# Kernel tuning notes

Measured on AMD Instinct MI355X. Metric: run time of the kernel, lower is better.

## Reference

```python
import jax, jax.numpy as jnp
import numpy as np


def _segment_mean(msg, dst, num_nodes):
    # msg: [E, B, O, T] summed into [N, B, O, T], mean over incoming edges
    s = jax.ops.segment_sum(msg, dst, num_segments=num_nodes)
    cnt = jax.ops.segment_sum(jnp.ones((msg.shape[0],), msg.dtype), dst, num_segments=num_nodes)
    return s / jnp.clip(cnt, 1.0)[:, None, None, None]


def _gcn(x, edge_index, edge_attr, A, Wk, Wr, b):
    # Edge-conditioned (spline-style) graph conv.
    # x: [B, N, Cin, T]; edge_attr: [E, 3]; Wk: [K, Cin, Cout]
    N = x.shape[1]
    src, dst = edge_index[0], edge_index[1]
    Bw = jax.nn.softmax(edge_attr @ A, axis=-1)          # [E, K] basis weights
    We = jnp.einsum('ek,kio->eio', Bw, Wk)                # [E, Cin, Cout]
    msg = jnp.einsum('beit,eio->ebot', x[:, src], We)     # [E, B, Cout, T]
    agg = _segment_mean(msg, dst, N).transpose(1, 0, 2, 3)  # [B, N, Cout, T]
    out = agg + jnp.einsum('bnit,io->bnot', x, Wr) + b[None, None, :, None]
    return jax.nn.elu(out)


def _pool(x, P, C, T):
    # x: [B, N_l, C, T] -> flatten, sparse-pool with P [N_{l+1}, N_l], unflatten
    B, N = x.shape[0], x.shape[1]
    xf = x.reshape(B, N, C * T)
    xf = jnp.einsum('mn,bnf->bmf', P, xf)
    return xf.reshape(B, P.shape[0], C, T)


def setup_inputs() -> dict:
    key = jax.random.key(0)
    ks = jax.random.split(key, 24)
    B, T = 2, 200
    N = [2048, 512, 128, 64]
    E = [16384, 8192, 2048]
    nf = [1, 8, 16, 32, 64, 128, 128]
    ld = 64

    def rn(k, shape, scale=1.0):
        return jax.random.normal(k, shape, dtype=jnp.float32) * scale

    inp = {}
    inp['x'] = rn(ks[0], (B, N[0], nf[0], T))
    inp['ei0'] = jax.random.randint(ks[1], (2, E[0]), 0, N[0])
    inp['ea0'] = jax.random.uniform(ks[2], (E[0], 3), dtype=jnp.float32)
    inp['ei1'] = jax.random.randint(ks[3], (2, E[1]), 0, N[1])
    inp['ea1'] = jax.random.uniform(ks[4], (E[1], 3), dtype=jnp.float32)
    inp['ei2'] = jax.random.randint(ks[5], (2, E[2]), 0, N[2])
    inp['ea2'] = jax.random.uniform(ks[6], (E[2], 3), dtype=jnp.float32)
    # gcn params: (A basis map, K=3 kernel weights, root weight, bias)
    inp['A1'] = rn(ks[7], (3, 3))
    inp['Wk1'] = rn(ks[8], (3, nf[0], nf[2]), 1.0 / np.sqrt(nf[0]))
    inp['Wr1'] = rn(ks[9], (nf[0], nf[2]), 1.0 / np.sqrt(nf[0]))
    inp['b1'] = jnp.zeros((nf[2],), jnp.float32)
    inp['A2'] = rn(ks[10], (3, 3))
    inp['Wk2'] = rn(ks[11], (3, nf[2], nf[3]), 1.0 / np.sqrt(nf[2]))
    inp['Wr2'] = rn(ks[12], (nf[2], nf[3]), 1.0 / np.sqrt(nf[2]))
    inp['b2'] = jnp.zeros((nf[3],), jnp.float32)
    inp['A3'] = rn(ks[13], (3, 3))
    inp['Wk3'] = rn(ks[14], (3, nf[3], nf[4]), 1.0 / np.sqrt(nf[3]))
    inp['Wr3'] = rn(ks[15], (nf[3], nf[4]), 1.0 / np.sqrt(nf[3]))
    inp['b3'] = jnp.zeros((nf[4],), jnp.float32)
    # sparse pooling projections (dense here)
    inp['P01'] = rn(ks[16], (N[1], N[0]), 1.0 / np.sqrt(N[0]))
    inp['P12'] = rn(ks[17], (N[2], N[1]), 1.0 / np.sqrt(N[1]))
    inp['P23'] = rn(ks[18], (N[3], N[2]), 1.0 / np.sqrt(N[2]))
    # 1x1 conv encoder head
    inp['fce1_w'] = rn(ks[19], (nf[4], nf[6]), 1.0 / np.sqrt(nf[4]))
    inp['fce1_b'] = jnp.zeros((nf[6],), jnp.float32)
    inp['fce2_w'] = rn(ks[20], (nf[6], ld), 1.0 / np.sqrt(nf[6]))
    inp['fce2_b'] = jnp.zeros((ld,), jnp.float32)
    return inp


def reference(x, ei0, ea0, ei1, ea1, ei2, ea2, A1, Wk1, Wr1, b1, A2, Wk2, Wr2, b2,
              A3, Wk3, Wr3, b3, P01, P12, P23, fce1_w, fce1_b, fce2_w, fce2_b):
    T = x.shape[-1]
    # level 0 -> 1
    h = _gcn(x, ei0, ea0, A1, Wk1, Wr1, b1)          # [B, N0, 16, T]
    h = _pool(h, P01, h.shape[2], T)                 # [B, N1, 16, T]
    # level 1 -> 2
    h = _gcn(h, ei1, ea1, A2, Wk2, Wr2, b2)          # [B, N1, 32, T]
    h = _pool(h, P12, h.shape[2], T)                 # [B, N2, 32, T]
    # level 2 -> 3
    h = _gcn(h, ei2, ea2, A3, Wk3, Wr3, b3)          # [B, N2, 64, T]
    h = _pool(h, P23, h.shape[2], T)                 # [B, N3, 64, T]
    # 1x1 conv encoder head (channel-wise linear over node/time grid)
    h = jax.nn.elu(jnp.einsum('bnct,co->bnot', h, fce1_w) + fce1_b[None, None, :, None])
    mu = jnp.tanh(jnp.einsum('bnct,co->bnot', h, fce2_w) + fce2_b[None, None, :, None])
    return mu  # [B, N3, latent_dim, T]
```

## Files before the change

kernel.cpp:

```cpp
#include <hip/hip_runtime.h>
#include <hip/hip_bf16.h>

using bf16 = __hip_bfloat16;
typedef unsigned short ushort_t;
typedef unsigned int uint_t;

constexpr int B = 2, T = 200;
constexpr int N0 = 2048, N1 = 512, N2 = 128, N3 = 64;
constexpr int E0 = 16384, E1 = 8192, E2 = 2048;

typedef __attribute__((ext_vector_type(8))) short bf16x8;
typedef __attribute__((ext_vector_type(4))) float f32x4;

__device__ __forceinline__ float ldx(const void* p, long i, int bf) {
  if (bf) {
    uint_t v = (uint_t)(((const ushort_t*)p)[i]) << 16;
    float f; __builtin_memcpy(&f, &v, 4); return f;
  }
  return ((const float*)p)[i];
}
__device__ __forceinline__ float rdf(const float* p) { return *p; }
__device__ __forceinline__ float rdf(const bf16* p) { return __bfloat162float(*p); }
__device__ __forceinline__ void stf(float* p, float v) { *p = v; }
__device__ __forceinline__ void stf(bf16* p, float v) { *p = __float2bfloat16(v); }
__device__ __forceinline__ ushort_t f2bfu(float v) {
  bf16 h = __float2bfloat16(v); ushort_t u; __builtin_memcpy(&u, &h, 2); return u;
}
__device__ __forceinline__ ushort_t ldbf(const bf16* p) { ushort_t u; __builtin_memcpy(&u, p, 2); return u; }
__device__ __forceinline__ ushort_t ldbf(const float* p) { return f2bfu(*p); }

__global__ void k_zero_ints(int* p, int n) {
  int i = blockIdx.x * 256 + threadIdx.x;
  if (i < n) p[i] = 0;
}

__global__ void k_probe(const ushort_t* ea, int* flag) {
  if (threadIdx.x == 0 && blockIdx.x == 0) {
    int c = 0;
    for (int i = 0; i < 128; ++i) {
      uint_t v = (uint_t)ea[i] << 16;
      float f; __builtin_memcpy(&f, &v, 4);
      if (f >= 0.f && f <= 1.0f) c++;
    }
    *flag = (c >= 120) ? 1 : 0;
  }
}

__global__ void k_cvtall(const void* x, const void* Wk1, const void* Wr1,
                         const void* Wk2, const void* Wr2,
                         const void* Wk3, const void* Wr3,
                         const void* W1h, const void* W2h,
                         const void* b1, const void* b2, const void* b3,
                         const void* b1h, const void* b2h,
                         const void* A1, const void* A2, const void* A3,
                         float* dst, const int* flagp) {
  int i = blockIdx.x * 256 + threadIdx.x;
  int bf = *flagp;
  if (i < 819200)       dst[i] = ldx(x,   i, bf);
  else if (i < 819248)  dst[i] = ldx(Wk1, i - 819200, bf);
  else if (i < 819264)  dst[i] = ldx(Wr1, i - 819248, bf);
  else if (i < 820800)  dst[i] = ldx(Wk2, i - 819264, bf);
  else if (i < 821312)  dst[i] = ldx(Wr2, i - 820800, bf);
  else if (i < 827456)  dst[i] = ldx(Wk3, i - 821312, bf);
  else if (i < 829504)  dst[i] = ldx(Wr3, i - 827456, bf);
  else if (i < 837696)  dst[i] = ldx(W1h, i - 829504, bf);
  else if (i < 845888)  dst[i] = ldx(W2h, i - 837696, bf);
  else if (i < 845904)  dst[i] = ldx(b1,  i - 845888, bf);
  else if (i < 845936)  dst[i] = ldx(b2,  i - 845904, bf);
  else if (i < 846000)  dst[i] = ldx(b3,  i - 845936, bf);
  else if (i < 846128)  dst[i] = ldx(b1h, i - 846000, bf);
  else if (i < 846192)  dst[i] = ldx(b2h, i - 846128, bf);
  else if (i < 846201)  dst[i] = ldx(A1,  i - 846192, bf);
  else if (i < 846210)  dst[i] = ldx(A2,  i - 846201, bf);
  else if (i < 846219)  dst[i] = ldx(A3,  i - 846210, bf);
}

__global__ void k_wprep(const float* wc2, const float* wc3, const float* w1h, const float* w2h,
                        ushort_t* t2, ushort_t* t3, ushort_t* t1h, ushort_t* t2h) {
  int i = blockIdx.x * 256 + threadIdx.x;
  if (i < 2048) { int o = i >> 6, c = i & 63; t2[i] = f2bfu(wc2[c * 32 + o]); }
  else if (i < 10240) { int j = i - 2048; int o = j >> 7, c = j & 127; t3[j] = f2bfu(wc3[c * 64 + o]); }
  else if (i < 18432) { int j = i - 10240; int o = j >> 6, c = j & 63; t1h[j] = f2bfu(w1h[c * 128 + o]); }
  else if (i < 26624) { int j = i - 18432; int o = j >> 7, c = j & 127; t2h[j] = f2bfu(w2h[c * 64 + o]); }
}

__global__ void k_hist3(const int* d0, const int* d1, const int* d2,
                        int* c0, int* c1, int* c2) {
  int i = blockIdx.x * 256 + threadIdx.x;
  if (i < E0) atomicAdd(&c0[d0[i]], 1);
  if (i < E1) atomicAdd(&c1[d1[i]], 1);
  if (i < E2) atomicAdd(&c2[d2[i]], 1);
}

__global__ void k_scan3(const int* c0, int* o0, int* u0,
                        const int* c1, int* o1, int* u1,
                        const int* c2, int* o2, int* u2) {
  const int* cnt; int* off; int* cur; int N;
  if (blockIdx.x == 0)      { cnt = c0; off = o0; cur = u0; N = N0; }
  else if (blockIdx.x == 1) { cnt = c1; off = o1; cur = u1; N = N1; }
  else                      { cnt = c2; off = o2; cur = u2; N = N2; }
  int tid = threadIdx.x;
  int chunk = (N + 63) >> 6;
  int base = tid * chunk;
  int s = 0;
  for (int j = 0; j < chunk; ++j) { int idx = base + j; if (idx < N) s += cnt[idx]; }
  int pre = s;
  for (int d = 1; d < 64; d <<= 1) {
    int v = __shfl_up(pre, d, 64);
    if (tid >= d) pre += v;
  }
  int run = pre - s;
  for (int j = 0; j < chunk; ++j) {
    int idx = base + j;
    if (idx < N) { off[idx] = run; cur[idx] = run; run += cnt[idx]; }
  }
  if (tid == 63) off[N] = run;
}

__global__ void k_fill3(const int* d0, int* u0, int* e0l,
                        const int* d1, int* u1, int* e1l,
                        const int* d2, int* u2, int* e2l) {
  int i = blockIdx.x * 256 + threadIdx.x;
  if (i < E0) { int p = atomicAdd(&u0[d0[i]], 1); e0l[p] = i; }
  if (i < E1) { int p = atomicAdd(&u1[d1[i]], 1); e1l[p] = i; }
  if (i < E2) { int p = atomicAdd(&u2[d2[i]], 1); e2l[p] = i; }
}

__device__ __forceinline__ void bw_one(const void* ea, int bf, const float* A,
                                       float* bw, int e) {
  float a0 = ldx(ea, e*3+0, bf), a1 = ldx(ea, e*3+1, bf), a2 = ldx(ea, e*3+2, bf);
  float l0 = a0*A[0] + a1*A[3] + a2*A[6];
  float l1 = a0*A[1] + a1*A[4] + a2*A[7];
  float l2 = a0*A[2] + a1*A[5] + a2*A[8];
  float m = fmaxf(l0, fmaxf(l1, l2));
  float x0 = expf(l0 - m), x1 = expf(l1 - m), x2 = expf(l2 - m);
  float inv = 1.0f / (x0 + x1 + x2);
  bw[e*3+0] = x0*inv; bw[e*3+1] = x1*inv; bw[e*3+2] = x2*inv;
}

__global__ void k_bw3(const void* ea0, const void* ea1, const void* ea2,
                      const float* Am, float* bw0, float* bw1, float* bw2,
                      const int* flagp) {
  int bf = *flagp;
  int i = blockIdx.x * 256 + threadIdx.x;
  if (i < E0) bw_one(ea0, bf, Am + 0,  bw0, i);
  if (i < E1) bw_one(ea1, bf, Am + 9,  bw1, i);
  if (i < E2) bw_one(ea2, bf, Am + 18, bw2, i);
}

__global__ void k_pcvt(const void* P01, const void* P12, const void* P23,
                       ushort_t* p1, ushort_t* p2, ushort_t* p3, const int* flagp) {
  int bf = *flagp;
  int i = blockIdx.x * 256 + threadIdx.x;
  if (i < 512 * 2048) p1[i] = f2bfu(ldx(P01, i, bf));
  if (i < 128 * 512)  p2[i] = f2bfu(ldx(P12, i, bf));
  if (i < 64 * 128)   p3[i] = f2bfu(ldx(P23, i, bf));
}

__global__ __launch_bounds__(256) void k_gc1(const float* x, const int* src,
    const int* off, const int* elist, const int* cnt, const float* bw,
    const float* W, const float* bias, bf16* h1) {
  __shared__ float Wl[64];
  __shared__ float bl[16];
  int tid = threadIdx.x;
  if (tid < 64) Wl[tid] = W[tid];
  if (tid < 16) bl[tid] = bias[tid];
  __syncthreads();
  int n = blockIdx.y, b = blockIdx.z;
  int t = tid;
  if (t >= T) return;
  int beg = off[n], end = off[n + 1];
  float a0 = 0.f, a1 = 0.f, a2 = 0.f;
  for (int q = beg; q < end; ++q) {
    int e = elist[q];
    int s = src[e];
    float xv = x[(b * N0 + s) * T + t];
    a0 += bw[e*3+0] * xv; a1 += bw[e*3+1] * xv; a2 += bw[e*3+2] * xv;
  }
  int c = cnt[n];
  float inv = 1.f / (float)(c > 0 ? c : 1);
  a0 *= inv; a1 *= inv; a2 *= inv;
  float xr = x[(b * N0 + n) * T + t];
  bf16* op = h1 + ((long)(b * N0 + n) * 16) * T + t;
#pragma unroll
  for (int o = 0; o < 16; ++o) {
    float v = a0 * Wl[o] + a1 * Wl[16 + o] + a2 * Wl[32 + o] + xr * Wl[48 + o] + bl[o];
    v = v > 0.f ? v : (expf(v) - 1.f);
    op[o * T] = __float2bfloat16(v);
  }
}

template<int CIN, int CPI, typename TOut>
__global__ __launch_bounds__(256) void k_gather(const float* x, const int* src,
    const int* off, const int* elist, const int* cnt, const float* bw,
    TOut* zx, int N) {
  int tx = threadIdx.x & 63, iy = threadIdx.x >> 6;
  int t = blockIdx.x * 64 + tx;
  int n = blockIdx.y, b = blockIdx.z;
  if (t >= T) return;
  int beg = off[n], end = off[n + 1];
  float acc[3][CPI];
#pragma unroll
  for (int k = 0; k < 3; ++k)
#pragma unroll
    for (int j = 0; j < CPI; ++j) acc[k][j] = 0.f;
  for (int q = beg; q < end; ++q) {
    int e = elist[q];
    int s = src[e];
    float w0 = bw[e*3+0], w1 = bw[e*3+1], w2 = bw[e*3+2];
    const float* xp = x + ((long)(b * N + s) * CIN) * T + t;
#pragma unroll
    for (int j = 0; j < CPI; ++j) {
      int i = iy * CPI + j;
      float xv = xp[i * T];
      acc[0][j] += w0 * xv; acc[1][j] += w1 * xv; acc[2][j] += w2 * xv;
    }
  }
  int c = cnt[n];
  float inv = 1.f / (float)(c > 0 ? c : 1);
  TOut* zp = zx + ((long)(b * N + n) * 4 * CIN) * T + t;
  const float* xs = x + ((long)(b * N + n) * CIN) * T + t;
#pragma unroll
  for (int j = 0; j < CPI; ++j) {
    int i = iy * CPI + j;
    stf(zp + (0 * CIN + i) * T, acc[0][j] * inv);
    stf(zp + (1 * CIN + i) * T, acc[1][j] * inv);
    stf(zp + (2 * CIN + i) * T, acc[2][j] * inv);
    stf(zp + (3 * CIN + i) * T, xs[i * T]);
  }
}

template<int C, int O, int ACT, typename TIn, int OUTM>
__global__ __launch_bounds__(256) void k_cmixm(const TIn* in, const ushort_t* Wt,
    const float* bias, void* outp, int N, const int* flagp) {
  constexpr int KG = C / 8;
  constexpr int MT = O / 16;
  __shared__ __align__(16) ushort_t Ws[O * C];
  __shared__ __align__(16) ushort_t Is[64 * C];
  int tid = threadIdx.x;
  int w = tid >> 6, l = tid & 63;
  int lf = l & 15, quad = l >> 4;
  int t0 = blockIdx.x * 64;
  int n = blockIdx.y, b = blockIdx.z;

  {
    const uint4* Wg = (const uint4*)Wt;
    for (int s = tid; s < O * KG; s += 256) {
      int o = s / KG, kg = s % KG;
      uint4 v = Wg[s];
      *(uint4*)(Ws + o * C + ((kg ^ (o & 7)) * 8)) = v;
    }
  }
  {
    const TIn* ip = in + ((long)(b * N + n) * C) * T + t0;
    int t = tid & 63;
    bool tok = (t0 + t) < T;
    for (int kg = tid >> 6; kg < KG; kg += 4) {
      ushort_t r[8];
#pragma unroll
      for (int j = 0; j < 8; ++j)
        r[j] = tok ? ldbf(ip + (kg * 8 + j) * T + t) : (ushort_t)0;
      *(uint4*)(Is + t * C + ((kg ^ (t & 7)) * 8)) = *(uint4*)r;
    }
  }
  __syncthreads();

  f32x4 acc[MT];
#pragma unroll
  for (int mt = 0; mt < MT; ++mt) acc[mt] = (f32x4){0.f, 0.f, 0.f, 0.f};
  int tr = w * 16 + lf;
#pragma unroll
  for (int kc = 0; kc < C / 32; ++kc) {
    int kg0 = kc * 4 + quad;
    bf16x8 bfr = *(const bf16x8*)(Is + tr * C + ((kg0 ^ (tr & 7)) * 8));
#pragma unroll
    for (int mt = 0; mt < MT; ++mt) {
      int o = mt * 16 + lf;
      bf16x8 afr = *(const bf16x8*)(Ws + o * C + ((kg0 ^ (o & 7)) * 8));
      acc[mt] = __builtin_amdgcn_mfma_f32_16x16x32_bf16(afr, bfr, acc[mt], 0, 0, 0);
    }
  }
  int t = t0 + w * 16 + lf;
  if (t < T) {
    long nb = (long)(b * N + n) * O;
    int bfflag = OUTM ? *flagp : 1;
#pragma unroll
    for (int mt = 0; mt < MT; ++mt) {
#pragma unroll
      for (int r = 0; r < 4; ++r) {
        int o = mt * 16 + quad * 4 + r;
        float v = acc[mt][r] + bias[o];
        if (ACT == 0) v = v > 0.f ? v : (expf(v) - 1.f);
        else          v = tanhf(v);
        long idx = (nb + o) * T + t;
        if (OUTM == 0) ((bf16*)outp)[idx] = __float2bfloat16(v);
        else if (bfflag) ((bf16*)outp)[idx] = __float2bfloat16(v);
        else ((float*)outp)[idx] = v;
      }
    }
  }
}

template<int WMT, typename TOut>
__global__ __launch_bounds__(256) void k_pool_mfma(const ushort_t* Pb, const ushort_t* h,
                                                   TOut* out, int M, int K, int F) {
  constexpr int BM = 64 * WMT;
  __shared__ __align__(16) ushort_t As[BM * 64];
  __shared__ __align__(16) ushort_t Bs[64 * 64];
  int tid = threadIdx.x;
  int w = tid >> 6, l = tid & 63;
  int lf = l & 15, quad = l >> 4;
  int f0 = blockIdx.x * 64;
  int m0 = blockIdx.y * BM;
  int b = blockIdx.z;
  f32x4 acc[WMT][4];
#pragma unroll
  for (int wt = 0; wt < WMT; ++wt)
#pragma unroll
    for (int ft = 0; ft < 4; ++ft) acc[wt][ft] = (f32x4){0.f, 0.f, 0.f, 0.f};

  for (int k0 = 0; k0 < K; k0 += 64) {
#pragma unroll
    for (int it = 0; it < BM / 32; ++it) {
      int cc = tid + 256 * it;
      int m = cc >> 3, kc = cc & 7;
      uint4 v = *(const uint4*)(Pb + (long)(m0 + m) * K + k0 + kc * 8);
      *(uint4*)(As + m * 64 + ((kc ^ (m & 7)) * 8)) = v;
    }
    {
      int f = tid & 63, kb = (tid >> 6) * 16;
      const ushort_t* hp = h + ((long)(b * K + k0 + kb)) * F + f0 + f;
      ushort_t r[16];
#pragma unroll
      for (int i = 0; i < 16; ++i) r[i] = hp[(long)i * F];
      int kc0 = kb >> 3;
      *(uint4*)(Bs + f * 64 + ((kc0 ^ (f & 7)) * 8)) = *(uint4*)&r[0];
      *(uint4*)(Bs + f * 64 + (((kc0 + 1) ^ (f & 7)) * 8)) = *(uint4*)&r[8];
    }
    __syncthreads();
#pragma unroll
    for (int ks = 0; ks < 2; ++ks) {
      int kc = ks * 4 + quad;
      bf16x8 bfr[4];
#pragma unroll
      for (int ft = 0; ft < 4; ++ft) {
        int fl = ft * 16 + lf;
        bfr[ft] = *(const bf16x8*)(Bs + fl * 64 + ((kc ^ (fl & 7)) * 8));
      }
#pragma unroll
      for (int wt = 0; wt < WMT; ++wt) {
        int ml = wt * 64 + w * 16 + lf;
        bf16x8 afr = *(const bf16x8*)(As + ml * 64 + ((kc ^ (ml & 7)) * 8));
#pragma unroll
        for (int ft = 0; ft < 4; ++ft)
          acc[wt][ft] = __builtin_amdgcn_mfma_f32_16x16x32_bf16(afr, bfr[ft], acc[wt][ft], 0, 0, 0);
      }
    }
    __syncthreads();
  }
#pragma unroll
  for (int wt = 0; wt < WMT; ++wt) {
#pragma unroll
    for (int r = 0; r < 4; ++r) {
      int m = m0 + wt * 64 + w * 16 + quad * 4 + r;
      TOut* op = out + ((long)(b * M + m)) * F + f0 + lf;
#pragma unroll
      for (int ft = 0; ft < 4; ++ft)
        stf(op + ft * 16, acc[wt][ft][r]);
    }
  }
}

extern "C" void kernel_launch(void* const* d_in, const int* in_sizes, int n_in,
                              void* d_out, int out_size, void* d_ws, size_t ws_size,
                              hipStream_t stream) {
  const int* ei0 = (const int*)d_in[1];
  const int* ei1 = (const int*)d_in[3];
  const int* ei2 = (const int*)d_in[5];

  char* base = (char*)d_ws;
  int* I = (int*)base;
  int* cnt0 = I;         int* off0 = I + 2048;  int* cur0 = I + 4112;  int* el0 = I + 6160;
  int* cnt1 = I + 22544; int* off1 = I + 23056; int* cur1 = I + 23584; int* el1 = I + 24096;
  int* cnt2 = I + 32288; int* off2 = I + 32416; int* cur2 = I + 32560; int* el2 = I + 32688;
  int* flagp = I + 40448;
  float* Fb = (float*)(base + 163840);
  float* xc  = Fb + 0;
  float* wc1 = Fb + 819200;
  float* wc2 = Fb + 819264;
  float* wc3 = Fb + 821312;
  float* w1h = Fb + 829504;
  float* w2h = Fb + 837696;
  float* bias= Fb + 845888;
  float* Am  = Fb + 846192;
  float* bw0 = Fb + 846220;
  float* bw1 = Fb + 895372;
  float* bw2 = Fb + 919948;
  ushort_t* Pb1 = (ushort_t*)(Fb + 926092);
  ushort_t* Pb2 = (ushort_t*)(Fb + 1450380);
  ushort_t* Pb3 = (ushort_t*)(Fb + 1483148);
  ushort_t* wt2  = (ushort_t*)(Fb + 1487244);
  ushort_t* wt3  = (ushort_t*)(Fb + 1488268);
  ushort_t* wt1h = (ushort_t*)(Fb + 1492364);
  ushort_t* wt2h = (ushort_t*)(Fb + 1496460);
  char* Aa = base + 8357888;
  char* Bb = base + 21465088;

  k_zero_ints<<<160, 256, 0, stream>>>(I, 40960);
  k_probe<<<1, 64, 0, stream>>>((const ushort_t*)d_in[2], flagp);
  k_cvtall<<<3306, 256, 0, stream>>>(d_in[0], d_in[8], d_in[9], d_in[12], d_in[13],
                                     d_in[16], d_in[17], d_in[22], d_in[24],
                                     d_in[10], d_in[14], d_in[18], d_in[23], d_in[25],
                                     d_in[7], d_in[11], d_in[15], Fb, flagp);
  k_hist3<<<64, 256, 0, stream>>>(ei0 + E0, ei1 + E1, ei2 + E2, cnt0, cnt1, cnt2);
  k_scan3<<<3, 64, 0, stream>>>(cnt0, off0, cur0, cnt1, off1, cur1, cnt2, off2, cur2);
  k_fill3<<<64, 256, 0, stream>>>(ei0 + E0, cur0, el0, ei1 + E1, cur1, el1, ei2 + E2, cur2, el2);
  k_bw3<<<64, 256, 0, stream>>>(d_in[2], d_in[4], d_in[6], Am, bw0, bw1, bw2, flagp);
  k_pcvt<<<4096, 256, 0, stream>>>(d_in[19], d_in[20], d_in[21], Pb1, Pb2, Pb3, flagp);
  k_wprep<<<104, 256, 0, stream>>>(wc2, wc3, w1h, w2h, wt2, wt3, wt1h, wt2h);

  k_gc1<<<dim3(1, N0, B), 256, 0, stream>>>(xc, ei0, off0, el0, cnt0, bw0, wc1, bias + 0, (bf16*)Bb);
  k_pool_mfma<2, float><<<dim3(50, 4, B), 256, 0, stream>>>(Pb1, (const ushort_t*)Bb, (float*)Aa, 512, 2048, 3200);
  k_gather<16, 4, bf16><<<dim3(4, N1, B), 256, 0, stream>>>((const float*)Aa, ei1, off1, el1, cnt1, bw1, (bf16*)Bb, N1);
  k_cmixm<64, 32, 0, bf16, 0><<<dim3(4, N1, B), 256, 0, stream>>>((const bf16*)Bb, wt2, bias + 16, Aa, N1, flagp);
  k_pool_mfma<1, float><<<dim3(100, 2, B), 256, 0, stream>>>(Pb2, (const ushort_t*)Aa, (float*)Bb, 128, 512, 6400);
  k_gather<32, 8, bf16><<<dim3(4, N2, B), 256, 0, stream>>>((const float*)Bb, ei2, off2, el2, cnt2, bw2, (bf16*)Aa, N2);
  k_cmixm<128, 64, 0, bf16, 0><<<dim3(4, N2, B), 256, 0, stream>>>((const bf16*)Aa, wt3, bias + 48, Bb, N2, flagp);
  k_pool_mfma<1, float><<<dim3(200, 1, B), 256, 0, stream>>>(Pb3, (const ushort_t*)Bb, (float*)Aa, 64, 128, 12800);
  k_cmixm<64, 128, 0, float, 0><<<dim3(4, N3, B), 256, 0, stream>>>((const float*)Aa, wt1h, bias + 112, Bb, N3, flagp);
  k_cmixm<128, 64, 1, bf16, 1><<<dim3(4, N3, B), 256, 0, stream>>>((const bf16*)Bb, wt2h, bias + 240, d_out, N3, flagp);
}
```

Before: 331.4 us.

## Fuse prep kernels, gather with channel mix, and both head layers

Merges the zeroing, probe, conversion, basis-weight, pool-matrix and weight-transpose launches into two setup kernels, and drops the separate fp32 copy of x by reading the input directly in the first conv. Each gather stage and its channel-mix MFMA become one kernel that builds the bf16 operand tile in shared memory, so the intermediate zx tensor is never written to global memory. The two head linears are fused into one kernel that keeps the hidden activations in shared memory. The first pool widens its F tile to 128. This cuts launches and global round trips, but the fused kernels use more shared memory and registers, which may lower occupancy.

```diff
diff --git a/kernel.cpp b/kernel.cpp
--- a/kernel.cpp
+++ b/kernel.cpp
@@ -11,6 +11,22 @@
 
 typedef __attribute__((ext_vector_type(8))) short bf16x8;
 typedef __attribute__((ext_vector_type(4))) float f32x4;
+
+constexpr size_t O_FLAG = 161792;
+constexpr size_t O_WC1  = 163840;
+constexpr size_t O_BIAS = 164096;
+constexpr size_t O_BW0  = 165312;
+constexpr size_t O_BW1  = 361920;
+constexpr size_t O_BW2  = 460224;
+constexpr size_t O_PB1  = 484800;
+constexpr size_t O_PB2  = 2581952;
+constexpr size_t O_PB3  = 2713024;
+constexpr size_t O_WT2  = 2729408;
+constexpr size_t O_WT3  = 2733504;
+constexpr size_t O_W1H  = 2749888;
+constexpr size_t O_W2H  = 2766272;
+constexpr size_t O_AA   = 2785280;
+constexpr size_t O_BB   = 15892480;
 
 __device__ __forceinline__ float ldx(const void* p, long i, int bf) {
   if (bf) {
@@ -19,69 +35,87 @@
   }
   return ((const float*)p)[i];
 }
-__device__ __forceinline__ float rdf(const float* p) { return *p; }
-__device__ __forceinline__ float rdf(const bf16* p) { return __bfloat162float(*p); }
 __device__ __forceinline__ void stf(float* p, float v) { *p = v; }
 __device__ __forceinline__ void stf(bf16* p, float v) { *p = __float2bfloat16(v); }
 __device__ __forceinline__ ushort_t f2bfu(float v) {
   bf16 h = __float2bfloat16(v); ushort_t u; __builtin_memcpy(&u, &h, 2); return u;
 }
-__device__ __forceinline__ ushort_t ldbf(const bf16* p) { ushort_t u; __builtin_memcpy(&u, p, 2); return u; }
-__device__ __forceinline__ ushort_t ldbf(const float* p) { return f2bfu(*p); }
-
-__global__ void k_zero_ints(int* p, int n) {
-  int i = blockIdx.x * 256 + threadIdx.x;
-  if (i < n) p[i] = 0;
-}
-
-__global__ void k_probe(const ushort_t* ea, int* flag) {
-  if (threadIdx.x == 0 && blockIdx.x == 0) {
+
+struct InPtrs {
+  const void* ea0; const void* ea1; const void* ea2;
+  const void* P01; const void* P12; const void* P23;
+  const void* Wk1; const void* Wr1; const void* Wk2; const void* Wr2;
+  const void* Wk3; const void* Wr3; const void* W1h; const void* W2h;
+  const void* b1; const void* b2; const void* b3; const void* b1h; const void* b2h;
+  const void* A1; const void* A2; const void* A3;
+};
+
+__global__ void k_setup0(int* I, const ushort_t* ea) {
+  if (blockIdx.x < 158) {
+    int i = blockIdx.x * 256 + threadIdx.x;
+    I[i] = 0;
+  } else if (threadIdx.x == 0) {
     int c = 0;
     for (int i = 0; i < 128; ++i) {
       uint_t v = (uint_t)ea[i] << 16;
       float f; __builtin_memcpy(&f, &v, 4);
       if (f >= 0.f && f <= 1.0f) c++;
     }
-    *flag = (c >= 120) ? 1 : 0;
-  }
-}
-
-__global__ void k_cvtall(const void* x, const void* Wk1, const void* Wr1,
-                         const void* Wk2, const void* Wr2,
-                         const void* Wk3, const void* Wr3,
-                         const void* W1h, const void* W2h,
-                         const void* b1, const void* b2, const void* b3,
-                         const void* b1h, const void* b2h,
-                         const void* A1, const void* A2, const void* A3,
-                         float* dst, const int* flagp) {
-  int i = blockIdx.x * 256 + threadIdx.x;
-  int bf = *flagp;
-  if (i < 819200)       dst[i] = ldx(x,   i, bf);
-  else if (i < 819248)  dst[i] = ldx(Wk1, i - 819200, bf);
-  else if (i < 819264)  dst[i] = ldx(Wr1, i - 819248, bf);
-  else if (i < 820800)  dst[i] = ldx(Wk2, i - 819264, bf);
-  else if (i < 821312)  dst[i] = ldx(Wr2, i - 820800, bf);
-  else if (i < 827456)  dst[i] = ldx(Wk3, i - 821312, bf);
-  else if (i < 829504)  dst[i] = ldx(Wr3, i - 827456, bf);
-  else if (i < 837696)  dst[i] = ldx(W1h, i - 829504, bf);
-  else if (i < 845888)  dst[i] = ldx(W2h, i - 837696, bf);
-  else if (i < 845904)  dst[i] = ldx(b1,  i - 845888, bf);
-  else if (i < 845936)  dst[i] = ldx(b2,  i - 845904, bf);
-  else if (i < 846000)  dst[i] = ldx(b3,  i - 845936, bf);
-  else if (i < 846128)  dst[i] = ldx(b1h, i - 846000, bf);
-  else if (i < 846192)  dst[i] = ldx(b2h, i - 846128, bf);
-  else if (i < 846201)  dst[i] = ldx(A1,  i - 846192, bf);
-  else if (i < 846210)  dst[i] = ldx(A2,  i - 846201, bf);
-  else if (i < 846219)  dst[i] = ldx(A3,  i - 846210, bf);
-}
-
-__global__ void k_wprep(const float* wc2, const float* wc3, const float* w1h, const float* w2h,
-                        ushort_t* t2, ushort_t* t3, ushort_t* t1h, ushort_t* t2h) {
-  int i = blockIdx.x * 256 + threadIdx.x;
-  if (i < 2048) { int o = i >> 6, c = i & 63; t2[i] = f2bfu(wc2[c * 32 + o]); }
-  else if (i < 10240) { int j = i - 2048; int o = j >> 7, c = j & 127; t3[j] = f2bfu(wc3[c * 64 + o]); }
-  else if (i < 18432) { int j = i - 10240; int o = j >> 6, c = j & 63; t1h[j] = f2bfu(w1h[c * 128 + o]); }
-  else if (i < 26624) { int j = i - 18432; int o = j >> 7, c = j & 127; t2h[j] = f2bfu(w2h[c * 64 + o]); }
+    *(int*)((char*)I + O_FLAG) = (c >= 120) ? 1 : 0;
+  }
+}
+
+__device__ __forceinline__ void bw_one(const void* ea, int bf, const void* A,
+                                       float* bw, int e) {
+  float a0 = ldx(ea, e*3+0, bf), a1 = ldx(ea, e*3+1, bf), a2 = ldx(ea, e*3+2, bf);
+  float l0 = a0*ldx(A,0,bf) + a1*ldx(A,3,bf) + a2*ldx(A,6,bf);
+  float l1 = a0*ldx(A,1,bf) + a1*ldx(A,4,bf) + a2*ldx(A,7,bf);
+  float l2 = a0*ldx(A,2,bf) + a1*ldx(A,5,bf) + a2*ldx(A,8,bf);
+  float m = fmaxf(l0, fmaxf(l1, l2));
+  float x0 = expf(l0 - m), x1 = expf(l1 - m), x2 = expf(l2 - m);
+  float inv = 1.0f / (x0 + x1 + x2);
+  bw[e*3+0] = x0*inv; bw[e*3+1] = x1*inv; bw[e*3+2] = x2*inv;
+}
+
+__global__ void k_prep(InPtrs P, char* base) {
+  int bf = *(const int*)(base + O_FLAG);
+  int bx = blockIdx.x, tid = threadIdx.x;
+  float* bw0 = (float*)(base + O_BW0);
+  float* bw1 = (float*)(base + O_BW1);
+  float* bw2 = (float*)(base + O_BW2);
+  if (bx < 64)        { bw_one(P.ea0, bf, P.A1, bw0, bx*256+tid); return; }
+  if (bx < 96)        { bw_one(P.ea1, bf, P.A2, bw1, (bx-64)*256+tid); return; }
+  if (bx < 104)       { bw_one(P.ea2, bf, P.A3, bw2, (bx-96)*256+tid); return; }
+  if (bx < 4200)      { long i = (long)(bx-104)*256+tid;
+                        ((ushort_t*)(base+O_PB1))[i] = f2bfu(ldx(P.P01, i, bf)); return; }
+  if (bx < 4456)      { int i = (bx-4200)*256+tid;
+                        ((ushort_t*)(base+O_PB2))[i] = f2bfu(ldx(P.P12, i, bf)); return; }
+  if (bx < 4488)      { int i = (bx-4456)*256+tid;
+                        ((ushort_t*)(base+O_PB3))[i] = f2bfu(ldx(P.P23, i, bf)); return; }
+  if (bx < 4496)      { int j = (bx-4488)*256+tid; int o = j>>6, c = j&63;
+                        float v = (c<48) ? ldx(P.Wk2, c*32+o, bf) : ldx(P.Wr2, (c-48)*32+o, bf);
+                        ((ushort_t*)(base+O_WT2))[j] = f2bfu(v); return; }
+  if (bx < 4528)      { int j = (bx-4496)*256+tid; int o = j>>7, c = j&127;
+                        float v = (c<96) ? ldx(P.Wk3, c*64+o, bf) : ldx(P.Wr3, (c-96)*64+o, bf);
+                        ((ushort_t*)(base+O_WT3))[j] = f2bfu(v); return; }
+  if (bx < 4560)      { int j = (bx-4528)*256+tid; int o = j>>6, c = j&63;
+                        ((ushort_t*)(base+O_W1H))[j] = f2bfu(ldx(P.W1h, c*128+o, bf)); return; }
+  if (bx < 4592)      { int j = (bx-4560)*256+tid; int o = j>>7, c = j&127;
+                        ((ushort_t*)(base+O_W2H))[j] = f2bfu(ldx(P.W2h, c*64+o, bf)); return; }
+  {
+    int i = (bx-4592)*256+tid;
+    if (i < 64) {
+      ((float*)(base+O_WC1))[i] = (i<48) ? ldx(P.Wk1, i, bf) : ldx(P.Wr1, i-48, bf);
+    } else if (i < 368) {
+      int j = i - 64; float v;
+      if (j < 16)       v = ldx(P.b1, j, bf);
+      else if (j < 48)  v = ldx(P.b2, j-16, bf);
+      else if (j < 112) v = ldx(P.b3, j-48, bf);
+      else if (j < 240) v = ldx(P.b1h, j-112, bf);
+      else              v = ldx(P.b2h, j-240, bf);
+      ((float*)(base+O_BIAS))[j] = v;
+    }
+  }
 }
 
 __global__ void k_hist3(const int* d0, const int* d1, const int* d2,
@@ -126,46 +160,16 @@
   if (i < E2) { int p = atomicAdd(&u2[d2[i]], 1); e2l[p] = i; }
 }
 
-__device__ __forceinline__ void bw_one(const void* ea, int bf, const float* A,
-                                       float* bw, int e) {
-  float a0 = ldx(ea, e*3+0, bf), a1 = ldx(ea, e*3+1, bf), a2 = ldx(ea, e*3+2, bf);
-  float l0 = a0*A[0] + a1*A[3] + a2*A[6];
-  float l1 = a0*A[1] + a1*A[4] + a2*A[7];
-  float l2 = a0*A[2] + a1*A[5] + a2*A[8];
-  float m = fmaxf(l0, fmaxf(l1, l2));
-  float x0 = expf(l0 - m), x1 = expf(l1 - m), x2 = expf(l2 - m);
-  float inv = 1.0f / (x0 + x1 + x2);
-  bw[e*3+0] = x0*inv; bw[e*3+1] = x1*inv; bw[e*3+2] = x2*inv;
-}
-
-__global__ void k_bw3(const void* ea0, const void* ea1, const void* ea2,
-                      const float* Am, float* bw0, float* bw1, float* bw2,
-                      const int* flagp) {
-  int bf = *flagp;
-  int i = blockIdx.x * 256 + threadIdx.x;
-  if (i < E0) bw_one(ea0, bf, Am + 0,  bw0, i);
-  if (i < E1) bw_one(ea1, bf, Am + 9,  bw1, i);
-  if (i < E2) bw_one(ea2, bf, Am + 18, bw2, i);
-}
-
-__global__ void k_pcvt(const void* P01, const void* P12, const void* P23,
-                       ushort_t* p1, ushort_t* p2, ushort_t* p3, const int* flagp) {
-  int bf = *flagp;
-  int i = blockIdx.x * 256 + threadIdx.x;
-  if (i < 512 * 2048) p1[i] = f2bfu(ldx(P01, i, bf));
-  if (i < 128 * 512)  p2[i] = f2bfu(ldx(P12, i, bf));
-  if (i < 64 * 128)   p3[i] = f2bfu(ldx(P23, i, bf));
-}
-
-__global__ __launch_bounds__(256) void k_gc1(const float* x, const int* src,
+__global__ __launch_bounds__(256) void k_gc1(const void* x, const int* src,
     const int* off, const int* elist, const int* cnt, const float* bw,
-    const float* W, const float* bias, bf16* h1) {
+    const float* W, const float* bias, bf16* h1, const int* flagp) {
   __shared__ float Wl[64];
   __shared__ float bl[16];
   int tid = threadIdx.x;
   if (tid < 64) Wl[tid] = W[tid];
   if (tid < 16) bl[tid] = bias[tid];
   __syncthreads();
+  int bf = *flagp;
   int n = blockIdx.y, b = blockIdx.z;
   int t = tid;
   if (t >= T) return;
@@ -174,13 +178,13 @@
   for (int q = beg; q < end; ++q) {
     int e = elist[q];
     int s = src[e];
-    float xv = x[(b * N0 + s) * T + t];
+    float xv = ldx(x, (long)(b * N0 + s) * T + t, bf);
     a0 += bw[e*3+0] * xv; a1 += bw[e*3+1] * xv; a2 += bw[e*3+2] * xv;
   }
   int c = cnt[n];
   float inv = 1.f / (float)(c > 0 ? c : 1);
   a0 *= inv; a1 *= inv; a2 *= inv;
-  float xr = x[(b * N0 + n) * T + t];
+  float xr = ldx(x, (long)(b * N0 + n) * T + t, bf);
   bf16* op = h1 + ((long)(b * N0 + n) * 16) * T + t;
 #pragma unroll
   for (int o = 0; o < 16; ++o) {
@@ -190,49 +194,11 @@
   }
 }
 
-template<int CIN, int CPI, typename TOut>
-__global__ __launch_bounds__(256) void k_gather(const float* x, const int* src,
+template<int CIN, int CPI, int O>
+__global__ __launch_bounds__(256) void k_gcm(const float* hp, const int* src,
     const int* off, const int* elist, const int* cnt, const float* bw,
-    TOut* zx, int N) {
-  int tx = threadIdx.x & 63, iy = threadIdx.x >> 6;
-  int t = blockIdx.x * 64 + tx;
-  int n = blockIdx.y, b = blockIdx.z;
-  if (t >= T) return;
-  int beg = off[n], end = off[n + 1];
-  float acc[3][CPI];
-#pragma unroll
-  for (int k = 0; k < 3; ++k)
-#pragma unroll
-    for (int j = 0; j < CPI; ++j) acc[k][j] = 0.f;
-  for (int q = beg; q < end; ++q) {
-    int e = elist[q];
-    int s = src[e];
-    float w0 = bw[e*3+0], w1 = bw[e*3+1], w2 = bw[e*3+2];
-    const float* xp = x + ((long)(b * N + s) * CIN) * T + t;
-#pragma unroll
-    for (int j = 0; j < CPI; ++j) {
-      int i = iy * CPI + j;
-      float xv = xp[i * T];
-      acc[0][j] += w0 * xv; acc[1][j] += w1 * xv; acc[2][j] += w2 * xv;
-    }
-  }
-  int c = cnt[n];
-  float inv = 1.f / (float)(c > 0 ? c : 1);
-  TOut* zp = zx + ((long)(b * N + n) * 4 * CIN) * T + t;
-  const float* xs = x + ((long)(b * N + n) * CIN) * T + t;
-#pragma unroll
-  for (int j = 0; j < CPI; ++j) {
-    int i = iy * CPI + j;
-    stf(zp + (0 * CIN + i) * T, acc[0][j] * inv);
-    stf(zp + (1 * CIN + i) * T, acc[1][j] * inv);
-    stf(zp + (2 * CIN + i) * T, acc[2][j] * inv);
-    stf(zp + (3 * CIN + i) * T, xs[i * T]);
-  }
-}
-
-template<int C, int O, int ACT, typename TIn, int OUTM>
-__global__ __launch_bounds__(256) void k_cmixm(const TIn* in, const ushort_t* Wt,
-    const float* bias, void* outp, int N, const int* flagp) {
+    const ushort_t* Wt, const float* bias, bf16* h, int N) {
+  constexpr int C = 4 * CIN;
   constexpr int KG = C / 8;
   constexpr int MT = O / 16;
   __shared__ __align__(16) ushort_t Ws[O * C];
@@ -242,32 +208,58 @@
   int lf = l & 15, quad = l >> 4;
   int t0 = blockIdx.x * 64;
   int n = blockIdx.y, b = blockIdx.z;
-
   {
     const uint4* Wg = (const uint4*)Wt;
     for (int s = tid; s < O * KG; s += 256) {
       int o = s / KG, kg = s % KG;
-      uint4 v = Wg[s];
-      *(uint4*)(Ws + o * C + ((kg ^ (o & 7)) * 8)) = v;
-    }
-  }
-  {
-    const TIn* ip = in + ((long)(b * N + n) * C) * T + t0;
-    int t = tid & 63;
-    bool tok = (t0 + t) < T;
-    for (int kg = tid >> 6; kg < KG; kg += 4) {
-      ushort_t r[8];
-#pragma unroll
-      for (int j = 0; j < 8; ++j)
-        r[j] = tok ? ldbf(ip + (kg * 8 + j) * T + t) : (ushort_t)0;
-      *(uint4*)(Is + t * C + ((kg ^ (t & 7)) * 8)) = *(uint4*)r;
-    }
+      *(uint4*)(Ws + o * C + ((kg ^ (o & 7)) * 8)) = Wg[s];
+    }
+  }
+  int tx = tid & 63, iy = tid >> 6;
+  int t = t0 + tx;
+  bool tok = t < T;
+  float acc[3][CPI], xr[CPI];
+#pragma unroll
+  for (int k = 0; k < 3; ++k)
+#pragma unroll
+    for (int j = 0; j < CPI; ++j) acc[k][j] = 0.f;
+#pragma unroll
+  for (int j = 0; j < CPI; ++j) xr[j] = 0.f;
+  float inv = 1.f;
+  if (tok) {
+    int beg = off[n], end = off[n + 1];
+    for (int q = beg; q < end; ++q) {
+      int e = elist[q];
+      int s = src[e];
+      float w0 = bw[e*3+0], w1 = bw[e*3+1], w2 = bw[e*3+2];
+      const float* xp = hp + ((long)(b * N + s) * CIN) * T + t;
+#pragma unroll
+      for (int j = 0; j < CPI; ++j) {
+        float xv = xp[(iy * CPI + j) * T];
+        acc[0][j] += w0 * xv; acc[1][j] += w1 * xv; acc[2][j] += w2 * xv;
+      }
+    }
+    int c = cnt[n];
+    inv = 1.f / (float)(c > 0 ? c : 1);
+    const float* xs = hp + ((long)(b * N + n) * CIN) * T + t;
+#pragma unroll
+    for (int j = 0; j < CPI; ++j) xr[j] = xs[(iy * CPI + j) * T];
+  }
+#pragma unroll
+  for (int j = 0; j < CPI; ++j) {
+    int i = iy * CPI + j;
+#pragma unroll
+    for (int k = 0; k < 3; ++k) {
+      int c = k * CIN + i;
+      Is[tx * C + ((c >> 3) ^ (tx & 7)) * 8 + (c & 7)] = f2bfu(acc[k][j] * inv);
+    }
+    int c = 3 * CIN + i;
+    Is[tx * C + ((c >> 3) ^ (tx & 7)) * 8 + (c & 7)] = f2bfu(xr[j]);
   }
   __syncthreads();
-
-  f32x4 acc[MT];
-#pragma unroll
-  for (int mt = 0; mt < MT; ++mt) acc[mt] = (f32x4){0.f, 0.f, 0.f, 0.f};
+  f32x4 dacc[MT];
+#pragma unroll
+  for (int mt = 0; mt < MT; ++mt) dacc[mt] = (f32x4){0.f, 0.f, 0.f, 0.f};
   int tr = w * 16 + lf;
 #pragma unroll
   for (int kc = 0; kc < C / 32; ++kc) {
@@ -277,47 +269,43 @@
     for (int mt = 0; mt < MT; ++mt) {
       int o = mt * 16 + lf;
       bf16x8 afr = *(const bf16x8*)(Ws + o * C + ((kg0 ^ (o & 7)) * 8));
-      acc[mt] = __builtin_amdgcn_mfma_f32_16x16x32_bf16(afr, bfr, acc[mt], 0, 0, 0);
-    }
-  }
-  int t = t0 + w * 16 + lf;
-  if (t < T) {
+      dacc[mt] = __builtin_amdgcn_mfma_f32_16x16x32_bf16(afr, bfr, dacc[mt], 0, 0, 0);
+    }
+  }
+  int tg = t0 + w * 16 + lf;
+  if (tg < T) {
     long nb = (long)(b * N + n) * O;
-    int bfflag = OUTM ? *flagp : 1;
 #pragma unroll
     for (int mt = 0; mt < MT; ++mt) {
 #pragma unroll
       for (int r = 0; r < 4; ++r) {
         int o = mt * 16 + quad * 4 + r;
-        float v = acc[mt][r] + bias[o];
-        if (ACT == 0) v = v > 0.f ? v : (expf(v) - 1.f);
-        else          v = tanhf(v);
-        long idx = (nb + o) * T + t;
-        if (OUTM == 0) ((bf16*)outp)[idx] = __float2bfloat16(v);
-        else if (bfflag) ((bf16*)outp)[idx] = __float2bfloat16(v);
-        else ((float*)outp)[idx] = v;
-      }
-    }
-  }
-}
-
-template<int WMT, typename TOut>
+        float v = dacc[mt][r] + bias[o];
+        v = v > 0.f ? v : (expf(v) - 1.f);
+        h[(nb + o) * T + tg] = __float2bfloat16(v);
+      }
+    }
+  }
+}
+
+template<int WMT, int FT, typename TOut>
 __global__ __launch_bounds__(256) void k_pool_mfma(const ushort_t* Pb, const ushort_t* h,
                                                    TOut* out, int M, int K, int F) {
   constexpr int BM = 64 * WMT;
+  constexpr int BN = 16 * FT;
   __shared__ __align__(16) ushort_t As[BM * 64];
-  __shared__ __align__(16) ushort_t Bs[64 * 64];
+  __shared__ __align__(16) ushort_t Bs[BN * 64];
   int tid = threadIdx.x;
   int w = tid >> 6, l = tid & 63;
   int lf = l & 15, quad = l >> 4;
-  int f0 = blockIdx.x * 64;
+  int f0 = blockIdx.x * BN;
   int m0 = blockIdx.y * BM;
   int b = blockIdx.z;
-  f32x4 acc[WMT][4];
+  f32x4 acc[WMT][FT];
 #pragma unroll
   for (int wt = 0; wt < WMT; ++wt)
 #pragma unroll
-    for (int ft = 0; ft < 4; ++ft) acc[wt][ft] = (f32x4){0.f, 0.f, 0.f, 0.f};
+    for (int ft = 0; ft < FT; ++ft) acc[wt][ft] = (f32x4){0.f, 0.f, 0.f, 0.f};
 
   for (int k0 = 0; k0 < K; k0 += 64) {
 #pragma unroll
@@ -327,8 +315,9 @@
       uint4 v = *(const uint4*)(Pb + (long)(m0 + m) * K + k0 + kc * 8);
       *(uint4*)(As + m * 64 + ((kc ^ (m & 7)) * 8)) = v;
     }
-    {
-      int f = tid & 63, kb = (tid >> 6) * 16;
+#pragma unroll
+    for (int kb = (tid / BN) * 16; kb < 64; kb += (256 / BN) * 16) {
+      int f = tid % BN;
       const ushort_t* hp = h + ((long)(b * K + k0 + kb)) * F + f0 + f;
       ushort_t r[16];
 #pragma unroll
@@ -341,9 +330,9 @@
 #pragma unroll
     for (int ks = 0; ks < 2; ++ks) {
       int kc = ks * 4 + quad;
-      bf16x8 bfr[4];
-#pragma unroll
-      for (int ft = 0; ft < 4; ++ft) {
+      bf16x8 bfr[FT];
+#pragma unroll
+      for (int ft = 0; ft < FT; ++ft) {
         int fl = ft * 16 + lf;
         bfr[ft] = *(const bf16x8*)(Bs + fl * 64 + ((kc ^ (fl & 7)) * 8));
       }
@@ -352,7 +341,7 @@
         int ml = wt * 64 + w * 16 + lf;
         bf16x8 afr = *(const bf16x8*)(As + ml * 64 + ((kc ^ (ml & 7)) * 8));
 #pragma unroll
-        for (int ft = 0; ft < 4; ++ft)
+        for (int ft = 0; ft < FT; ++ft)
           acc[wt][ft] = __builtin_amdgcn_mfma_f32_16x16x32_bf16(afr, bfr[ft], acc[wt][ft], 0, 0, 0);
       }
     }
@@ -365,8 +354,107 @@
       int m = m0 + wt * 64 + w * 16 + quad * 4 + r;
       TOut* op = out + ((long)(b * M + m)) * F + f0 + lf;
 #pragma unroll
-      for (int ft = 0; ft < 4; ++ft)
+      for (int ft = 0; ft < FT; ++ft)
         stf(op + ft * 16, acc[wt][ft][r]);
+    }
+  }
+}
+
+__global__ __launch_bounds__(256) void k_head(const float* hp3, const ushort_t* W1t,
+    const ushort_t* W2t, const float* bias, void* outp, const int* flagp) {
+  __shared__ __align__(16) ushort_t Ws1[128 * 64];
+  __shared__ __align__(16) ushort_t Ws2[64 * 128];
+  __shared__ __align__(16) ushort_t Is[64 * 64];
+  __shared__ __align__(16) ushort_t G[64 * 128];
+  int tid = threadIdx.x;
+  int w = tid >> 6, l = tid & 63;
+  int lf = l & 15, quad = l >> 4;
+  int t0 = blockIdx.x * 64;
+  int n = blockIdx.y, b = blockIdx.z;
+  {
+    const uint4* g1 = (const uint4*)W1t;
+    for (int s = tid; s < 1024; s += 256) {
+      int o = s >> 3, kg = s & 7;
+      *(uint4*)(Ws1 + o * 64 + ((kg ^ (o & 7)) * 8)) = g1[s];
+    }
+    const uint4* g2 = (const uint4*)W2t;
+    for (int s = tid; s < 1024; s += 256) {
+      int o = s >> 4, kg = s & 15;
+      *(uint4*)(Ws2 + o * 128 + ((kg ^ (o & 7)) * 8)) = g2[s];
+    }
+  }
+  {
+    int t = tid & 63;
+    bool tok = (t0 + t) < T;
+    const float* ip = hp3 + ((long)(b * 64 + n) * 64) * T + t0;
+    for (int kg = tid >> 6; kg < 8; kg += 4) {
+      ushort_t r[8];
+#pragma unroll
+      for (int j = 0; j < 8; ++j)
+        r[j] = tok ? f2bfu(ip[(kg * 8 + j) * T + t]) : (ushort_t)0;
+      *(uint4*)(Is + t * 64 + ((kg ^ (t & 7)) * 8)) = *(uint4*)r;
+    }
+  }
+  __syncthreads();
+  int tr = w * 16 + lf;
+  {
+    f32x4 a1[8];
+#pragma unroll
+    for (int mt = 0; mt < 8; ++mt) a1[mt] = (f32x4){0.f, 0.f, 0.f, 0.f};
+#pragma unroll
+    for (int kc = 0; kc < 2; ++kc) {
+      int kg0 = kc * 4 + quad;
+      bf16x8 bfr = *(const bf16x8*)(Is + tr * 64 + ((kg0 ^ (tr & 7)) * 8));
+#pragma unroll
+      for (int mt = 0; mt < 8; ++mt) {
+        int o = mt * 16 + lf;
+        bf16x8 afr = *(const bf16x8*)(Ws1 + o * 64 + ((kg0 ^ (o & 7)) * 8));
+        a1[mt] = __builtin_amdgcn_mfma_f32_16x16x32_bf16(afr, bfr, a1[mt], 0, 0, 0);
+      }
+    }
+    int tG = w * 16 + lf;
+#pragma unroll
+    for (int mt = 0; mt < 8; ++mt) {
+#pragma unroll
+      for (int r = 0; r < 4; ++r) {
+        int o1 = mt * 16 + quad * 4 + r;
+        float v = a1[mt][r] + bias[112 + o1];
+        v = v > 0.f ? v : (expf(v) - 1.f);
+        G[tG * 128 + ((o1 >> 3) ^ (tG & 7)) * 8 + (o1 & 7)] = f2bfu(v);
+      }
+    }
+  }
+  __syncthreads();
+  {
+    f32x4 a2[4];
+#pragma unroll
+    for (int mt = 0; mt < 4; ++mt) a2[mt] = (f32x4){0.f, 0.f, 0.f, 0.f};
+#pragma unroll
+    for (int kc = 0; kc < 4; ++kc) {
+      int kg0 = kc * 4 + quad;
+      bf16x8 bfr = *(const bf16x8*)(G + tr * 128 + ((kg0 ^ (tr & 7)) * 8));
+#pragma unroll
+      for (int mt = 0; mt < 4; ++mt) {
+        int o = mt * 16 + lf;
+        bf16x8 afr = *(const bf16x8*)(Ws2 + o * 128 + ((kg0 ^ (o & 7)) * 8));
+        a2[mt] = __builtin_amdgcn_mfma_f32_16x16x32_bf16(afr, bfr, a2[mt], 0, 0, 0);
+      }
+    }
+    int t = t0 + w * 16 + lf;
+    if (t < T) {
+      int bf = *flagp;
+      long nb = (long)(b * 64 + n) * 64;
+#pragma unroll
+      for (int mt = 0; mt < 4; ++mt) {
+#pragma unroll
+        for (int r = 0; r < 4; ++r) {
+          int o2 = mt * 16 + quad * 4 + r;
+          float v = tanhf(a2[mt][r] + bias[240 + o2]);
+          long idx = (nb + o2) * T + t;
+          if (bf) ((bf16*)outp)[idx] = __float2bfloat16(v);
+          else    ((float*)outp)[idx] = v;
+        }
+      }
     }
   }
 }
@@ -383,50 +471,38 @@
   int* cnt0 = I;         int* off0 = I + 2048;  int* cur0 = I + 4112;  int* el0 = I + 6160;
   int* cnt1 = I + 22544; int* off1 = I + 23056; int* cur1 = I + 23584; int* el1 = I + 24096;
   int* cnt2 = I + 32288; int* off2 = I + 32416; int* cur2 = I + 32560; int* el2 = I + 32688;
-  int* flagp = I + 40448;
-  float* Fb = (float*)(base + 163840);
-  float* xc  = Fb + 0;
-  float* wc1 = Fb + 819200;
-  float* wc2 = Fb + 819264;
-  float* wc3 = Fb + 821312;
-  float* w1h = Fb + 829504;
-  float* w2h = Fb + 837696;
-  float* bias= Fb + 845888;
-  float* Am  = Fb + 846192;
-  float* bw0 = Fb + 846220;
-  float* bw1 = Fb + 895372;
-  float* bw2 = Fb + 919948;
-  ushort_t* Pb1 = (ushort_t*)(Fb + 926092);
-  ushort_t* Pb2 = (ushort_t*)(Fb + 1450380);
-  ushort_t* Pb3 = (ushort_t*)(Fb + 1483148);
-  ushort_t* wt2  = (ushort_t*)(Fb + 1487244);
-  ushort_t* wt3  = (ushort_t*)(Fb + 1488268);
-  ushort_t* wt1h = (ushort_t*)(Fb + 1492364);
-  ushort_t* wt2h = (ushort_t*)(Fb + 1496460);
-  char* Aa = base + 8357888;
-  char* Bb = base + 21465088;
-
-  k_zero_ints<<<160, 256, 0, stream>>>(I, 40960);
-  k_probe<<<1, 64, 0, stream>>>((const ushort_t*)d_in[2], flagp);
-  k_cvtall<<<3306, 256, 0, stream>>>(d_in[0], d_in[8], d_in[9], d_in[12], d_in[13],
-                                     d_in[16], d_in[17], d_in[22], d_in[24],
-                                     d_in[10], d_in[14], d_in[18], d_in[23], d_in[25],
-                                     d_in[7], d_in[11], d_in[15], Fb, flagp);
+  const int* flagp = (const int*)(base + O_FLAG);
+  float* wc1f = (float*)(base + O_WC1);
+  float* bias = (float*)(base + O_BIAS);
+  float* bw0 = (float*)(base + O_BW0);
+  float* bw1 = (float*)(base + O_BW1);
+  float* bw2 = (float*)(base + O_BW2);
+  ushort_t* Pb1 = (ushort_t*)(base + O_PB1);
+  ushort_t* Pb2 = (ushort_t*)(base + O_PB2);
+  ushort_t* Pb3 = (ushort_t*)(base + O_PB3);
+  ushort_t* wt2 = (ushort_t*)(base + O_WT2);
+  ushort_t* wt3 = (ushort_t*)(base + O_WT3);
+  ushort_t* w1t = (ushort_t*)(base + O_W1H);
+  ushort_t* w2t = (ushort_t*)(base + O_W2H);
+  char* Aa = base + O_AA;
+  char* Bb = base + O_BB;
+
+  InPtrs P = { d_in[2], d_in[4], d_in[6], d_in[19], d_in[20], d_in[21],
+               d_in[8], d_in[9], d_in[12], d_in[13], d_in[16], d_in[17],
+               d_in[22], d_in[24], d_in[10], d_in[14], d_in[18], d_in[23],
+               d_in[25], d_in[7], d_in[11], d_in[15] };
+
+  k_setup0<<<159, 256, 0, stream>>>(I, (const ushort_t*)d_in[2]);
+  k_prep<<<4594, 256, 0, stream>>>(P, base);
   k_hist3<<<64, 256, 0, stream>>>(ei0 + E0, ei1 + E1, ei2 + E2, cnt0, cnt1, cnt2);
   k_scan3<<<3, 64, 0, stream>>>(cnt0, off0, cur0, cnt1, off1, cur1, cnt2, off2, cur2);
   k_fill3<<<64, 256, 0, stream>>>(ei0 + E0, cur0, el0, ei1 + E1, cur1, el1, ei2 + E2, cur2, el2);
-  k_bw3<<<64, 256, 0, stream>>>(d_in[2], d_in[4], d_in[6], Am, bw0, bw1, bw2, flagp);
-  k_pcvt<<<4096, 256, 0, stream>>>(d_in[19], d_in[20], d_in[21], Pb1, Pb2, Pb3, flagp);
-  k_wprep<<<104, 256, 0, stream>>>(wc2, wc3, w1h, w2h, wt2, wt3, wt1h, wt2h);
-
-  k_gc1<<<dim3(1, N0, B), 256, 0, stream>>>(xc, ei0, off0, el0, cnt0, bw0, wc1, bias + 0, (bf16*)Bb);
-  k_pool_mfma<2, float><<<dim3(50, 4, B), 256, 0, stream>>>(Pb1, (const ushort_t*)Bb, (float*)Aa, 512, 2048, 3200);
-  k_gather<16, 4, bf16><<<dim3(4, N1, B), 256, 0, stream>>>((const float*)Aa, ei1, off1, el1, cnt1, bw1, (bf16*)Bb, N1);
-  k_cmixm<64, 32, 0, bf16, 0><<<dim3(4, N1, B), 256, 0, stream>>>((const bf16*)Bb, wt2, bias + 16, Aa, N1, flagp);
-  k_pool_mfma<1, float><<<dim3(100, 2, B), 256, 0, stream>>>(Pb2, (const ushort_t*)Aa, (float*)Bb, 128, 512, 6400);
-  k_gather<32, 8, bf16><<<dim3(4, N2, B), 256, 0, stream>>>((const float*)Bb, ei2, off2, el2, cnt2, bw2, (bf16*)Aa, N2);
-  k_cmixm<128, 64, 0, bf16, 0><<<dim3(4, N2, B), 256, 0, stream>>>((const bf16*)Aa, wt3, bias + 48, Bb, N2, flagp);
-  k_pool_mfma<1, float><<<dim3(200, 1, B), 256, 0, stream>>>(Pb3, (const ushort_t*)Bb, (float*)Aa, 64, 128, 12800);
-  k_cmixm<64, 128, 0, float, 0><<<dim3(4, N3, B), 256, 0, stream>>>((const float*)Aa, wt1h, bias + 112, Bb, N3, flagp);
-  k_cmixm<128, 64, 1, bf16, 1><<<dim3(4, N3, B), 256, 0, stream>>>((const bf16*)Bb, wt2h, bias + 240, d_out, N3, flagp);
-}
+
+  k_gc1<<<dim3(1, N0, B), 256, 0, stream>>>(d_in[0], ei0, off0, el0, cnt0, bw0, wc1f, bias, (bf16*)Bb, flagp);
+  k_pool_mfma<2, 8, float><<<dim3(25, 4, B), 256, 0, stream>>>(Pb1, (const ushort_t*)Bb, (float*)Aa, 512, 2048, 3200);
+  k_gcm<16, 4, 32><<<dim3(4, N1, B), 256, 0, stream>>>((const float*)Aa, ei1, off1, el1, cnt1, bw1, wt2, bias + 16, (bf16*)Bb, N1);
+  k_pool_mfma<1, 4, float><<<dim3(100, 2, B), 256, 0, stream>>>(Pb2, (const ushort_t*)Bb, (float*)Aa, 128, 512, 6400);
+  k_gcm<32, 8, 64><<<dim3(4, N2, B), 256, 0, stream>>>((const float*)Aa, ei2, off2, el2, cnt2, bw2, wt3, bias + 48, (bf16*)Bb, N2);
+  k_pool_mfma<1, 4, float><<<dim3(200, 1, B), 256, 0, stream>>>(Pb3, (const ushort_t*)Bb, (float*)Aa, 64, 128, 12800);
+  k_head<<<dim3(4, N3, B), 256, 0, stream>>>((const float*)Aa, w1t, w2t, bias, d_out, flagp);
+}
```

Result: no change. 334.0 us (+0.8%).
